# Kernel tuning notes

Hardware: AMD Instinct MI355X
Metric: run time of the kernel (lower is better)

## Reference

```python
import jax, jax.numpy as jnp
import numpy as np

N = 100000
E = 3200000
H = 16       # hidden_dim
D = 32       # decoder_dim
O = 2        # output_dim
EPS = 1e-5   # BatchNorm eps


def _xavier(key, out_f, in_f):
    limit = np.sqrt(6.0 / (in_f + out_f)).astype(np.float32)
    return jax.random.uniform(key, (out_f, in_f), jnp.float32, -limit, limit)


def setup_inputs() -> dict:
    key = jax.random.key(0)
    ks = jax.random.split(key, 24)
    inp = {
        'x': jax.random.normal(ks[0], (N, 1), jnp.float32),
        'edge_index': jax.random.randint(ks[1], (2, E), 0, N, jnp.int64),
        # SAGEConv1: in=1 -> out=H
        'W1l': _xavier(ks[2], H, 1), 'b1l': jnp.zeros((H,), jnp.float32), 'W1r': _xavier(ks[3], H, 1),
        # BatchNorm(hidden) running stats + affine (eval mode)
        'bn_gamma': jnp.ones((H,), jnp.float32), 'bn_beta': jnp.zeros((H,), jnp.float32),
        'bn_mean': jnp.zeros((H,), jnp.float32), 'bn_var': jnp.ones((H,), jnp.float32),
        # SAGEConv2/3: H -> H
        'W2l': _xavier(ks[4], H, H), 'b2l': jnp.zeros((H,), jnp.float32), 'W2r': _xavier(ks[5], H, H),
        'W3l': _xavier(ks[6], H, H), 'b3l': jnp.zeros((H,), jnp.float32), 'W3r': _xavier(ks[7], H, H),
        # SAGEConv4: H -> D
        'W4l': _xavier(ks[8], D, H), 'b4l': jnp.zeros((D,), jnp.float32), 'W4r': _xavier(ks[9], D, H),
        # decoder MLP
        'Wd1': _xavier(ks[10], D, D), 'bd1': jnp.zeros((D,), jnp.float32),
        'Wd2': _xavier(ks[11], O, D), 'bd2': jnp.zeros((O,), jnp.float32),
    }
    return inp


def _sage(x, src, dst, inv_cnt, Wl, bl, Wr):
    # mean-aggregate neighbor (source) features onto destination nodes
    msg = x[src]                                                  # [E, F]
    agg = jax.ops.segment_sum(msg, dst, num_segments=N) * inv_cnt  # [N, F]
    return agg @ Wl.T + bl + x @ Wr.T


def reference(x, edge_index, W1l, b1l, W1r, bn_gamma, bn_beta, bn_mean, bn_var,
              W2l, b2l, W2r, W3l, b3l, W3r, W4l, b4l, W4r, Wd1, bd1, Wd2, bd2):
    src, dst = edge_index[0], edge_index[1]
    cnt = jax.ops.segment_sum(jnp.ones((E,), jnp.float32), dst, num_segments=N)
    inv_cnt = (1.0 / jnp.maximum(cnt, 1.0))[:, None]              # [N, 1]

    h = _sage(x, src, dst, inv_cnt, W1l, b1l, W1r)
    # BatchNorm (eval mode: running stats) + ReLU
    h = (h - bn_mean) * jax.lax.rsqrt(bn_var + EPS) * bn_gamma + bn_beta
    h = jax.nn.relu(h)
    h = jax.nn.relu(_sage(h, src, dst, inv_cnt, W2l, b2l, W2r))
    h = jax.nn.relu(_sage(h, src, dst, inv_cnt, W3l, b3l, W3r))
    h = _sage(h, src, dst, inv_cnt, W4l, b4l, W4r)
    h = jax.nn.relu(h @ Wd1.T + bd1)
    h = h @ Wd2.T + bd2
    return jax.nn.softmax(h, axis=-1)
```

## Files before the change

kernel.cpp:

```cpp
#include <hip/hip_runtime.h>
#include <hip/hip_bf16.h>

#define EPS  1e-5f
#define SPAN 400
#define MAXB 256
#define PBE  2048
typedef __hip_bfloat16 bf16;
typedef int iv4 __attribute__((ext_vector_type(4)));
typedef int iv2 __attribute__((ext_vector_type(2)));

__global__ void k_hist(const int* __restrict__ dst, int* __restrict__ binCnt, int nE)
{
    __shared__ int hist[MAXB];
    int t = threadIdx.x;
    for (int k = t; k < MAXB; k += blockDim.x) hist[k] = 0;
    __syncthreads();
    int tid = blockIdx.x * blockDim.x + t;
    int stride = gridDim.x * blockDim.x;
    const iv4* d4 = (const iv4*)dst;
    int n4 = nE >> 2;
    for (int e = tid; e < n4; e += stride) {
        iv4 d = __builtin_nontemporal_load(&d4[e]);
        atomicAdd(&hist[d.x / SPAN], 1);
        atomicAdd(&hist[d.y / SPAN], 1);
        atomicAdd(&hist[d.z / SPAN], 1);
        atomicAdd(&hist[d.w / SPAN], 1);
    }
    if (blockIdx.x == 0 && t == 0)
        for (int e = n4 << 2; e < nE; ++e) atomicAdd(&hist[dst[e] / SPAN], 1);
    __syncthreads();
    for (int k = t; k < MAXB; k += blockDim.x)
        if (hist[k]) atomicAdd(&binCnt[k], hist[k]);
}

__global__ void k_binscan(const int* __restrict__ binCnt, int* __restrict__ binStart,
                          int* __restrict__ binCur, int nbins, int nE)
{
    __shared__ int ls[MAXB];
    int t = threadIdx.x;
    ls[t] = (t < nbins) ? binCnt[t] : 0;
    __syncthreads();
#pragma unroll
    for (int off = 1; off < MAXB; off <<= 1) {
        int u = (t >= off) ? ls[t - off] : 0;
        __syncthreads();
        ls[t] += u;
        __syncthreads();
    }
    int start = (t == 0) ? 0 : ls[t - 1];
    if (t < nbins) { binStart[t] = start; binCur[t] = start; }
    if (t == 0) binStart[nbins] = nE;
}

__global__ void k_pairs(const int* __restrict__ src, const int* __restrict__ dst,
                        int* __restrict__ binCur, iv2* __restrict__ stg, int nE)
{
    __shared__ int hist[MAXB], base[MAXB], cur[MAXB];
    int t = threadIdx.x;
    for (int k = t; k < MAXB; k += 256) { hist[k] = 0; cur[k] = 0; }
    __syncthreads();
    const iv4* d4 = (const iv4*)dst;
    const iv4* s4 = (const iv4*)src;
    int n4 = nE >> 2;
    int i0 = blockIdx.x * (PBE / 4) + 2 * t;
    bool v0 = i0 < n4, v1 = i0 + 1 < n4;
    iv4 d0 = {0,0,0,0}, s0 = {0,0,0,0}, d1 = {0,0,0,0}, s1 = {0,0,0,0};
    if (v0) { d0 = __builtin_nontemporal_load(&d4[i0]);     s0 = __builtin_nontemporal_load(&s4[i0]); }
    if (v1) { d1 = __builtin_nontemporal_load(&d4[i0 + 1]); s1 = __builtin_nontemporal_load(&s4[i0 + 1]); }
    if (v0) {
        atomicAdd(&hist[d0.x / SPAN], 1); atomicAdd(&hist[d0.y / SPAN], 1);
        atomicAdd(&hist[d0.z / SPAN], 1); atomicAdd(&hist[d0.w / SPAN], 1);
    }
    if (v1) {
        atomicAdd(&hist[d1.x / SPAN], 1); atomicAdd(&hist[d1.y / SPAN], 1);
        atomicAdd(&hist[d1.z / SPAN], 1); atomicAdd(&hist[d1.w / SPAN], 1);
    }
    bool tailblk = (blockIdx.x == gridDim.x - 1) && (t == 0);
    if (tailblk)
        for (int e = n4 << 2; e < nE; ++e) atomicAdd(&hist[dst[e] / SPAN], 1);
    __syncthreads();
    for (int k = t; k < MAXB; k += 256) {
        int tot = hist[k];
        base[k] = tot ? atomicAdd(&binCur[k], tot) : 0;
    }
    __syncthreads();
#define EMIT(dd, ss_) { int b = (dd) / SPAN; \
        int p = base[b] + atomicAdd(&cur[b], 1); \
        iv2 pr; pr.x = (dd); pr.y = (ss_); stg[p] = pr; }
    if (v0) { EMIT(d0.x, s0.x) EMIT(d0.y, s0.y) EMIT(d0.z, s0.z) EMIT(d0.w, s0.w) }
    if (v1) { EMIT(d1.x, s1.x) EMIT(d1.y, s1.y) EMIT(d1.z, s1.z) EMIT(d1.w, s1.w) }
    if (tailblk)
        for (int e = n4 << 2; e < nE; ++e) { EMIT(dst[e], src[e]) }
#undef EMIT
}

__global__ __launch_bounds__(1024) void k_sortbin(
    const iv2* __restrict__ stg, const int* __restrict__ binStart,
    int* __restrict__ rp, float* __restrict__ inv_cnt, int* __restrict__ csr,
    int n, int nbins)
{
    __shared__ int cnt[SPAN];
    __shared__ int cur[SPAN];
    __shared__ int ls[512];
    int t = threadIdx.x;
    int bin = blockIdx.x, lo = bin * SPAN;
    int nn = min(SPAN, n - lo);
    for (int k = t; k < SPAN; k += 1024) cnt[k] = 0;
    __syncthreads();
    int e0 = binStart[bin], e1 = binStart[bin + 1];
    for (int e = e0 + t; e < e1; e += 1024) {
        iv2 p = __builtin_nontemporal_load(&stg[e]);
        atomicAdd(&cnt[p.x - lo], 1);
    }
    __syncthreads();
    if (t < 512) ls[t] = (t < nn) ? cnt[t] : 0;
    __syncthreads();
#pragma unroll
    for (int off = 1; off < 512; off <<= 1) {
        int u = (t >= off && t < 512) ? ls[t - off] : 0;
        __syncthreads();
        if (t < 512) ls[t] += u;
        __syncthreads();
    }
    if (t < nn) {
        int c = cnt[t];
        int excl = ls[t] - c;
        cur[t] = excl;
        rp[lo + t] = e0 + excl;
        inv_cnt[lo + t] = 1.0f / fmaxf((float)c, 1.0f);
    }
    if (bin == nbins - 1 && t == 0) rp[n] = e1;
    __syncthreads();
    for (int e = e0 + t; e < e1; e += 1024) {
        iv2 p = __builtin_nontemporal_load(&stg[e]);
        int pos = atomicAdd(&cur[p.x - lo], 1);
        csr[e0 + pos] = p.y;
    }
}

__global__ void k_l1g(const int* __restrict__ rp, const int* __restrict__ csr,
                      const float* __restrict__ inv_cnt, const float* __restrict__ x,
                      const float* __restrict__ W1l, const float* __restrict__ b1l,
                      const float* __restrict__ W1r,
                      const float* __restrict__ gam, const float* __restrict__ bet,
                      const float* __restrict__ mu,  const float* __restrict__ var,
                      bf16* __restrict__ hout, int n)
{
    __shared__ float sWl[16], sb[16], sWr[16], ssc[16], sbi[16];
    int t = threadIdx.x;
    if (t < 16) {
        sWl[t] = W1l[t]; sb[t] = b1l[t]; sWr[t] = W1r[t];
        float sc = gam[t] * rsqrtf(var[t] + EPS);
        ssc[t] = sc;
        sbi[t] = bet[t] - mu[t] * sc;
    }
    __syncthreads();
    int grp = t >> 4, f = t & 15;
    int i = blockIdx.x * 16 + grp;
    if (i >= n) return;
    int r0 = rp[i], r1 = rp[i + 1];
    float s = 0.0f;
    for (int k = r0 + f; k < r1; k += 16) s += x[csr[k]];
#pragma unroll
    for (int m = 8; m >= 1; m >>= 1) s += __shfl_xor(s, m, 64);
    float mean = s * inv_cnt[i];
    float xv = x[i];
    float v = fmaf(mean, sWl[f], sb[f]);
    v = fmaf(xv, sWr[f], v);
    v = fmaxf(fmaf(v, ssc[f], sbi[f]), 0.0f);
    hout[(size_t)i * 16 + f] = __float2bfloat16(v);
}

__global__ void k_sage16(const int* __restrict__ rp, const int* __restrict__ csr,
                         const float* __restrict__ inv_cnt, const bf16* __restrict__ h,
                         const float* __restrict__ Wl, const float* __restrict__ bl,
                         const float* __restrict__ Wr,
                         bf16* __restrict__ hout, int n)
{
    __shared__ float sWlT[256], sWrT[256], sb[16];
    __shared__ float sA[16][17], sX[16][17];
    int t = threadIdx.x;
    {
        int j = t & 15, ii = t >> 4;
        sWlT[ii * 16 + j] = Wl[j * 16 + ii];
        sWrT[ii * 16 + j] = Wr[j * 16 + ii];
    }
    if (t < 16) sb[t] = bl[t];
    int grp = t >> 4, f = t & 15;
    int i = blockIdx.x * 16 + grp;
    bool valid = i < n;
    float acc = 0.0f, ic = 0.0f, hs = 0.0f;
    if (valid) {
        int r0 = rp[i], r1 = rp[i + 1];
#pragma unroll 4
        for (int k = r0; k < r1; ++k) {
            int nb = csr[k];
            acc += __bfloat162float(h[(size_t)nb * 16 + f]);
        }
        ic = inv_cnt[i];
        hs = __bfloat162float(h[(size_t)i * 16 + f]);
    }
    sA[grp][f] = acc * ic;
    sX[grp][f] = hs;
    __syncthreads();
    if (valid) {
        float o = sb[f];
#pragma unroll
        for (int ii = 0; ii < 16; ++ii) {
            o = fmaf(sA[grp][ii], sWlT[ii * 16 + f], o);
            o = fmaf(sX[grp][ii], sWrT[ii * 16 + f], o);
        }
        hout[(size_t)i * 16 + f] = __float2bfloat16(fmaxf(o, 0.0f));
    }
}

__global__ void k_fin(const int* __restrict__ rp, const int* __restrict__ csr,
                      const float* __restrict__ inv_cnt, const bf16* __restrict__ h,
                      const float* __restrict__ W4l, const float* __restrict__ b4l,
                      const float* __restrict__ W4r,
                      const float* __restrict__ Wd1, const float* __restrict__ bd1,
                      const float* __restrict__ Wd2, const float* __restrict__ bd2,
                      float* __restrict__ out, int n)
{
    __shared__ float sW4lT[512], sW4rT[512], sb4[32];
    __shared__ float sWd1T[1024], sbd1[32], sWd2[64], sbd2[2];
    __shared__ float sA[16][17], sX[16][17], sH4[16][33];
    int t = threadIdx.x;
    for (int k = t; k < 512; k += 256) {
        int j = k >> 4, ii = k & 15;
        sW4lT[ii * 32 + j] = W4l[k];
        sW4rT[ii * 32 + j] = W4r[k];
    }
    for (int k = t; k < 1024; k += 256) {
        int j = k >> 5, ii = k & 31;
        sWd1T[ii * 32 + j] = Wd1[k];
    }
    if (t < 32) { sb4[t] = b4l[t]; sbd1[t] = bd1[t]; }
    if (t < 64) sWd2[t] = Wd2[t];
    if (t < 2)  sbd2[t] = bd2[t];
    int grp = t >> 4, f = t & 15;
    int i = blockIdx.x * 16 + grp;
    bool valid = i < n;
    float acc = 0.0f, ic = 0.0f, hs = 0.0f;
    if (valid) {
        int r0 = rp[i], r1 = rp[i + 1];
#pragma unroll 4
        for (int k = r0; k < r1; ++k) {
            int nb = csr[k];
            acc += __bfloat162float(h[(size_t)nb * 16 + f]);
        }
        ic = inv_cnt[i];
        hs = __bfloat162float(h[(size_t)i * 16 + f]);
    }
    sA[grp][f] = acc * ic;
    sX[grp][f] = hs;
    __syncthreads();
    float h4a = sb4[f], h4b = sb4[f + 16];
#pragma unroll
    for (int ii = 0; ii < 16; ++ii) {
        float a  = sA[grp][ii];
        float xx = sX[grp][ii];
        h4a = fmaf(a,  sW4lT[ii * 32 + f],      h4a);
        h4b = fmaf(a,  sW4lT[ii * 32 + f + 16], h4b);
        h4a = fmaf(xx, sW4rT[ii * 32 + f],      h4a);
        h4b = fmaf(xx, sW4rT[ii * 32 + f + 16], h4b);
    }
    sH4[grp][f] = h4a;
    sH4[grp][f + 16] = h4b;
    __syncthreads();
    float za = sbd1[f], zb = sbd1[f + 16];
#pragma unroll
    for (int k = 0; k < 32; ++k) {
        float hv = sH4[grp][k];
        za = fmaf(hv, sWd1T[k * 32 + f],      za);
        zb = fmaf(hv, sWd1T[k * 32 + f + 16], zb);
    }
    za = fmaxf(za, 0.0f);
    zb = fmaxf(zb, 0.0f);
    float o0 = za * sWd2[f]      + zb * sWd2[f + 16];
    float o1 = za * sWd2[32 + f] + zb * sWd2[32 + f + 16];
#pragma unroll
    for (int m = 8; m >= 1; m >>= 1) {
        o0 += __shfl_xor(o0, m, 64);
        o1 += __shfl_xor(o1, m, 64);
    }
    if (valid && f == 0) {
        o0 += sbd2[0]; o1 += sbd2[1];
        float mx = fmaxf(o0, o1);
        float e0 = expf(o0 - mx), e1 = expf(o1 - mx);
        float inv = 1.0f / (e0 + e1);
        out[(size_t)2 * i + 0] = e0 * inv;
        out[(size_t)2 * i + 1] = e1 * inv;
    }
}

extern "C" void kernel_launch(void* const* d_in, const int* in_sizes, int n_in,
                              void* d_out, int out_size, void* d_ws, size_t ws_size,
                              hipStream_t stream)
{
    const float* x  = (const float*)d_in[0];
    const int*   ei = (const int*)d_in[1];
    const int    N  = in_sizes[0];
    const int    E  = in_sizes[1] / 2;
    const int* src = ei;
    const int* dst = ei + E;

    const float* W1l = (const float*)d_in[2];
    const float* b1l = (const float*)d_in[3];
    const float* W1r = (const float*)d_in[4];
    const float* gam = (const float*)d_in[5];
    const float* bet = (const float*)d_in[6];
    const float* mu  = (const float*)d_in[7];
    const float* var = (const float*)d_in[8];
    const float* W2l = (const float*)d_in[9];
    const float* b2l = (const float*)d_in[10];
    const float* W2r = (const float*)d_in[11];
    const float* W3l = (const float*)d_in[12];
    const float* b3l = (const float*)d_in[13];
    const float* W3r = (const float*)d_in[14];
    const float* W4l = (const float*)d_in[15];
    const float* b4l = (const float*)d_in[16];
    const float* W4r = (const float*)d_in[17];
    const float* Wd1 = (const float*)d_in[18];
    const float* bd1 = (const float*)d_in[19];
    const float* Wd2 = (const float*)d_in[20];
    const float* bd2 = (const float*)d_in[21];

    char*  base = (char*)d_ws;
    size_t off  = 0;
    auto alloc = [&](size_t bytes) { size_t p = off; off += (bytes + 63) & ~(size_t)63; return p; };
    float* inv_cnt  = (float*)(base + alloc((size_t)N * 4));
    int*   rp       = (int*)  (base + alloc((size_t)(N + 1) * 4));
    int*   binCnt   = (int*)  (base + alloc(MAXB * 4));
    int*   binStart = (int*)  (base + alloc((MAXB + 1) * 4));
    int*   binCur   = (int*)  (base + alloc(MAXB * 4));
    int*   csr      = (int*)  (base + alloc((size_t)E * 4));
    size_t regionOff = alloc((size_t)E * 8 > (size_t)N * 64 ? (size_t)E * 8 : (size_t)N * 64);
    iv2*   stg = (iv2*) (base + regionOff);
    bf16*  hA  = (bf16*)(base + regionOff);
    bf16*  hB  = hA + (size_t)N * 16;
    (void)ws_size;

    int nbins   = (N + SPAN - 1) / SPAN;
    int nbPairs = (E + PBE - 1) / PBE;
    int nbN16   = (N + 15) / 16;

    hipMemsetAsync(binCnt, 0, MAXB * sizeof(int), stream);
    k_hist<<<1024, 256, 0, stream>>>(dst, binCnt, E);
    k_binscan<<<1, 256, 0, stream>>>(binCnt, binStart, binCur, nbins, E);
    k_pairs<<<nbPairs, 256, 0, stream>>>(src, dst, binCur, stg, E);
    k_sortbin<<<nbins, 1024, 0, stream>>>(stg, binStart, rp, inv_cnt, csr, N, nbins);

    k_l1g<<<nbN16, 256, 0, stream>>>(rp, csr, inv_cnt, x, W1l, b1l, W1r,
                                     gam, bet, mu, var, hA, N);
    k_sage16<<<nbN16, 256, 0, stream>>>(rp, csr, inv_cnt, hA, W2l, b2l, W2r, hB, N);
    k_sage16<<<nbN16, 256, 0, stream>>>(rp, csr, inv_cnt, hB, W3l, b3l, W3r, hA, N);
    k_fin<<<nbN16, 256, 0, stream>>>(rp, csr, inv_cnt, hA, W4l, b4l, W4r,
                                     Wd1, bd1, Wd2, bd2, (float*)d_out, N);
}
```

Measured before the change: 257.1 us.

## Gather neighbor rows with 16-byte vector loads split across eight edge slots

Replaces the per-feature scalar gather loop in the middle SAGE layers and the final fused layer. Each group of 16 threads now splits into 8 edge slots times 2 halves. Every lane loads a 16-byte chunk of a neighbor's bf16 row, unpacks it by bit shifting, and the partial sums are reduced with xor shuffles. This cuts the serial per-node loop length and the number of memory instructions, at the cost of more registers and shuffle work. The weight transposes into shared memory in the final kernel are also reindexed so the shared-memory writes are contiguous.

```diff
diff --git a/kernel.cpp b/kernel.cpp
--- a/kernel.cpp
+++ b/kernel.cpp
@@ -8,6 +8,9 @@
 typedef __hip_bfloat16 bf16;
 typedef int iv4 __attribute__((ext_vector_type(4)));
 typedef int iv2 __attribute__((ext_vector_type(2)));
+
+__device__ __forceinline__ float bflo(unsigned u) { return __uint_as_float(u << 16); }
+__device__ __forceinline__ float bfhi(unsigned u) { return __uint_as_float(u & 0xffff0000u); }
 
 __global__ void k_hist(const int* __restrict__ dst, int* __restrict__ binCnt, int nE)
 {
@@ -171,6 +174,38 @@
     hout[(size_t)i * 16 + f] = __float2bfloat16(v);
 }
 
+__device__ __forceinline__ void gather8(const unsigned short* hu,
+                                        const int* __restrict__ csr,
+                                        int r0, int r1, bool valid,
+                                        int sl, int pr, float ic,
+                                        int lane16, float* sArow)
+{
+    float a0 = 0, a1 = 0, a2 = 0, a3 = 0, a4 = 0, a5 = 0, a6 = 0, a7 = 0;
+    if (valid) {
+        for (int k = r0 + sl; k < r1; k += 8) {
+            int nb = csr[k];
+            const uint4* rowp = (const uint4*)(hu + (size_t)nb * 16 + pr * 8);
+            uint4 u = *rowp;
+            a0 += bflo(u.x); a1 += bfhi(u.x);
+            a2 += bflo(u.y); a3 += bfhi(u.y);
+            a4 += bflo(u.z); a5 += bfhi(u.z);
+            a6 += bflo(u.w); a7 += bfhi(u.w);
+        }
+    }
+#pragma unroll
+    for (int m = 2; m <= 8; m <<= 1) {
+        a0 += __shfl_xor(a0, m, 64); a1 += __shfl_xor(a1, m, 64);
+        a2 += __shfl_xor(a2, m, 64); a3 += __shfl_xor(a3, m, 64);
+        a4 += __shfl_xor(a4, m, 64); a5 += __shfl_xor(a5, m, 64);
+        a6 += __shfl_xor(a6, m, 64); a7 += __shfl_xor(a7, m, 64);
+    }
+    if (valid && lane16 < 2) {
+        float* p = sArow + pr * 8;
+        p[0] = a0 * ic; p[1] = a1 * ic; p[2] = a2 * ic; p[3] = a3 * ic;
+        p[4] = a4 * ic; p[5] = a5 * ic; p[6] = a6 * ic; p[7] = a7 * ic;
+    }
+}
+
 __global__ void k_sage16(const int* __restrict__ rp, const int* __restrict__ csr,
                          const float* __restrict__ inv_cnt, const bf16* __restrict__ h,
                          const float* __restrict__ Wl, const float* __restrict__ bl,
@@ -187,21 +222,15 @@
     }
     if (t < 16) sb[t] = bl[t];
     int grp = t >> 4, f = t & 15;
+    int sl = f >> 1, pr = f & 1;
     int i = blockIdx.x * 16 + grp;
     bool valid = i < n;
-    float acc = 0.0f, ic = 0.0f, hs = 0.0f;
-    if (valid) {
-        int r0 = rp[i], r1 = rp[i + 1];
-#pragma unroll 4
-        for (int k = r0; k < r1; ++k) {
-            int nb = csr[k];
-            acc += __bfloat162float(h[(size_t)nb * 16 + f]);
-        }
-        ic = inv_cnt[i];
-        hs = __bfloat162float(h[(size_t)i * 16 + f]);
-    }
-    sA[grp][f] = acc * ic;
-    sX[grp][f] = hs;
+    const unsigned short* hu = (const unsigned short*)h;
+    int r0 = 0, r1 = 0;
+    float ic = 0.0f;
+    if (valid) { r0 = rp[i]; r1 = rp[i + 1]; ic = inv_cnt[i]; }
+    gather8(hu, csr, r0, r1, valid, sl, pr, ic, f, &sA[grp][0]);
+    if (valid) sX[grp][f] = __bfloat162float(h[(size_t)i * 16 + f]);
     __syncthreads();
     if (valid) {
         float o = sb[f];
@@ -227,33 +256,27 @@
     __shared__ float sA[16][17], sX[16][17], sH4[16][33];
     int t = threadIdx.x;
     for (int k = t; k < 512; k += 256) {
-        int j = k >> 4, ii = k & 15;
-        sW4lT[ii * 32 + j] = W4l[k];
-        sW4rT[ii * 32 + j] = W4r[k];
+        int ii = k >> 5, j = k & 31;
+        sW4lT[k] = W4l[j * 16 + ii];
+        sW4rT[k] = W4r[j * 16 + ii];
     }
     for (int k = t; k < 1024; k += 256) {
-        int j = k >> 5, ii = k & 31;
-        sWd1T[ii * 32 + j] = Wd1[k];
+        int ii = k >> 5, j = k & 31;
+        sWd1T[k] = Wd1[j * 32 + ii];
     }
     if (t < 32) { sb4[t] = b4l[t]; sbd1[t] = bd1[t]; }
     if (t < 64) sWd2[t] = Wd2[t];
     if (t < 2)  sbd2[t] = bd2[t];
     int grp = t >> 4, f = t & 15;
+    int sl = f >> 1, pr = f & 1;
     int i = blockIdx.x * 16 + grp;
     bool valid = i < n;
-    float acc = 0.0f, ic = 0.0f, hs = 0.0f;
-    if (valid) {
-        int r0 = rp[i], r1 = rp[i + 1];
-#pragma unroll 4
-        for (int k = r0; k < r1; ++k) {
-            int nb = csr[k];
-            acc += __bfloat162float(h[(size_t)nb * 16 + f]);
-        }
-        ic = inv_cnt[i];
-        hs = __bfloat162float(h[(size_t)i * 16 + f]);
-    }
-    sA[grp][f] = acc * ic;
-    sX[grp][f] = hs;
+    const unsigned short* hu = (const unsigned short*)h;
+    int r0 = 0, r1 = 0;
+    float ic = 0.0f;
+    if (valid) { r0 = rp[i]; r1 = rp[i + 1]; ic = inv_cnt[i]; }
+    gather8(hu, csr, r0, r1, valid, sl, pr, ic, f, &sA[grp][0]);
+    if (valid) sX[grp][f] = __bfloat162float(h[(size_t)i * 16 + f]);
     __syncthreads();
     float h4a = sb4[f], h4b = sb4[f + 16];
 #pragma unroll
```

After: 252.4 us. About the same (-1.8%).
